# Performance work log

Hardware: AMD Instinct MI355X
Metric: run time of the kernel (lower is better)

## Reference

```python
import jax, jax.numpy as jnp
import numpy as np
from jax import lax

IOU_THRESHOLD = 0.5
TOP = 1000


def setup_inputs() -> dict:
    key = jax.random.key(0)
    k1, k2, k3, k4, k5 = jax.random.split(key, 5)
    B, P = 16, 20000
    # valid (x1, y1, x2, y2) boxes on an ~800x800 image
    x1 = jax.random.uniform(k1, (B, P)) * 800.0
    y1 = jax.random.uniform(k2, (B, P)) * 800.0
    w = jax.random.uniform(k3, (B, P)) * 200.0 + 1.0
    h = jax.random.uniform(k4, (B, P)) * 200.0 + 1.0
    reg = jnp.stack([x1, y1, x1 + w, y1 + h], axis=-1)  # [B, P, 4]
    cls = jax.random.normal(k5, (B, P))                  # [B, P]
    return {"reg": reg, "cls": cls}


def _pairwise_iou(boxes):
    """boxes: [B, N, 4] (x1,y1,x2,y2) -> IoU [B, N, N]."""
    a = boxes[:, :, None, :]  # [B, N, 1, 4]
    b = boxes[:, None, :, :]  # [B, 1, N, 4]
    xx1 = jnp.maximum(a[..., 0], b[..., 0])
    yy1 = jnp.maximum(a[..., 1], b[..., 1])
    xx2 = jnp.minimum(a[..., 2], b[..., 2])
    yy2 = jnp.minimum(a[..., 3], b[..., 3])
    inter = jnp.clip(xx2 - xx1, 0.0) * jnp.clip(yy2 - yy1, 0.0)
    area_a = (a[..., 2] - a[..., 0]) * (a[..., 3] - a[..., 1])
    area_b = (b[..., 2] - b[..., 0]) * (b[..., 3] - b[..., 1])
    return inter / (area_a + area_b - inter)


def reference(reg, cls):
    B = cls.shape[0]
    # sort by confidence descending, gather boxes, keep top
    order = jnp.argsort(-cls, axis=1)                      # [B, P]
    sorted_cls = jnp.take_along_axis(cls, order, axis=1)[:, :TOP]            # [B, N]
    sorted_reg = jnp.take_along_axis(reg, order[:, :, None], axis=1)[:, :TOP]  # [B, N, 4]
    N = sorted_cls.shape[1]

    iou = _pairwise_iou(sorted_reg)                        # [B, N, N]

    # sequential greedy suppression: if box i still kept, drop boxes with IoU>=thr
    def body(mask, i):
        keep_i = mask[:, i]                                # [B]
        tmp = iou[:, i, :] < IOU_THRESHOLD                 # [B, N]
        upd = (mask & tmp).at[:, i].set(True)
        new_mask = jnp.where(keep_i[:, None], upd, mask)
        return new_mask, None

    mask0 = jnp.ones((B, N), dtype=bool)
    mask, _ = lax.scan(body, mask0, jnp.arange(N))

    out_reg = jnp.where(mask[:, :, None], sorted_reg, 0.0)
    out_cls = jnp.where(mask, sorted_cls, 0.0)
    return out_reg, out_cls
```

## Files before the change

### kernel.cpp

```cpp
#include <hip/hip_runtime.h>
#include <stdint.h>

#define BATCH 16
#define NPTS  20000
#define TOPK  1000

__device__ __forceinline__ uint32_t key_desc(float f) {
    uint32_t u = __float_as_uint(f);
    uint32_t m = (u & 0x80000000u) ? ~u : (u | 0x80000000u);
    return ~m;
}

__device__ __forceinline__ float key_undo(uint32_t k) {
    uint32_t m = ~k;
    uint32_t u = (m & 0x80000000u) ? (m & 0x7FFFFFFFu) : ~m;
    return __uint_as_float(u);
}

__device__ __forceinline__ void digit_find(const uint32_t* hist, int* sh_r,
                                           uint32_t* sh_pfx, int shift, int tid) {
    if (tid < 64) {
        int r = *sh_r;
        uint32_t v0 = hist[4 * tid + 0], v1 = hist[4 * tid + 1];
        uint32_t v2 = hist[4 * tid + 2], v3 = hist[4 * tid + 3];
        uint32_t s = v0 + v1 + v2 + v3;
        uint32_t x = s;
        #pragma unroll
        for (int d = 1; d < 64; d <<= 1) {
            uint32_t t = __shfl_up(x, d);
            if (tid >= d) x += t;
        }
        uint32_t e0 = x - s;
        uint32_t e1 = e0 + v0, e2 = e1 + v1, e3 = e2 + v2, e4 = e3 + v3;
        uint32_t ur = (uint32_t)r;
        if (ur >= e0 && ur < e4) {
            int digit; uint32_t eSel;
            if      (ur < e1) { digit = 4 * tid + 0; eSel = e0; }
            else if (ur < e2) { digit = 4 * tid + 1; eSel = e1; }
            else if (ur < e3) { digit = 4 * tid + 2; eSel = e2; }
            else              { digit = 4 * tid + 3; eSel = e3; }
            *sh_r = r - (int)eSel;
            *sh_pfx |= ((uint32_t)digit << shift);
        }
    }
}

__global__ __launch_bounds__(1024) void topk_kernel(
    const float* __restrict__ reg, const float* __restrict__ cls,
    float4* __restrict__ ws_boxes, float* __restrict__ ws_cls)
{
    __shared__ uint32_t whist[16][256];
    __shared__ uint32_t merged[256];
    __shared__ uint32_t sh_kpfx;
    __shared__ uint32_t sh_ipfx;
    __shared__ int      sh_r;
    __shared__ int      sh_cnt;
    __shared__ uint64_t sel[1024];

    const int b    = blockIdx.x;
    const int tid  = threadIdx.x;
    const int wave = tid >> 6;
    const float* c = cls + (size_t)b * NPTS;

    if (tid == 0) { sh_r = TOPK - 1; sh_kpfx = 0; sh_ipfx = 0; sh_cnt = 0; }

    uint32_t kreg[20];
    #pragma unroll
    for (int j = 0; j < 20; ++j) {
        int p = tid + j * 1024;
        kreg[j] = (p < NPTS) ? key_desc(c[p]) : 0xFFFFFFFFu;
    }
    __syncthreads();

    uint32_t kpfx = 0, kmask = 0;
    for (int pass = 0; pass < 4; ++pass) {
        for (int i = tid; i < 16 * 256; i += 1024) ((uint32_t*)whist)[i] = 0;
        __syncthreads();
        const int shift = 24 - 8 * pass;
        #pragma unroll
        for (int j = 0; j < 20; ++j) {
            int p = tid + j * 1024;
            uint32_t k = kreg[j];
            if (p < NPTS && (k & kmask) == kpfx)
                atomicAdd(&whist[wave][(k >> shift) & 255], 1u);
        }
        __syncthreads();
        if (tid < 256) {
            uint32_t s = 0;
            #pragma unroll
            for (int w2 = 0; w2 < 16; ++w2) s += whist[w2][tid];
            merged[tid] = s;
        }
        __syncthreads();
        digit_find(merged, &sh_r, &sh_kpfx, shift, tid);
        __syncthreads();
        kpfx = sh_kpfx;
        kmask |= (0xFFu << shift);
    }
    const uint32_t kth = kpfx;
    const uint32_t kthcnt = merged[kth & 255];

    uint32_t ipfx = 0;
    if (kthcnt > 1) {
        uint32_t imask = 0;
        for (int pass = 0; pass < 2; ++pass) {
            for (int i = tid; i < 16 * 256; i += 1024) ((uint32_t*)whist)[i] = 0;
            __syncthreads();
            const int shift = 8 - 8 * pass;
            #pragma unroll
            for (int j = 0; j < 20; ++j) {
                int p = tid + j * 1024;
                if (p < NPTS && kreg[j] == kth && (((uint32_t)p) & imask) == ipfx)
                    atomicAdd(&whist[wave][((uint32_t)p >> shift) & 255], 1u);
            }
            __syncthreads();
            if (tid < 256) {
                uint32_t s = 0;
                #pragma unroll
                for (int w2 = 0; w2 < 16; ++w2) s += whist[w2][tid];
                merged[tid] = s;
            }
            __syncthreads();
            digit_find(merged, &sh_r, &sh_ipfx, shift, tid);
            __syncthreads();
            ipfx = sh_ipfx;
            imask |= (0xFFu << shift);
        }
    } else {
        ipfx = 0xFFFFFFFFu;
    }
    const uint64_t kthkey = ((uint64_t)kth << 32) | (uint64_t)ipfx;

    sel[tid] = ~0ull;
    __syncthreads();
    #pragma unroll
    for (int j = 0; j < 20; ++j) {
        int p = tid + j * 1024;
        if (p < NPTS) {
            uint64_t key = ((uint64_t)kreg[j] << 32) | (uint32_t)p;
            if (key <= kthkey) {
                int pos = atomicAdd(&sh_cnt, 1);
                sel[pos] = key;
            }
        }
    }
    __syncthreads();

    uint64_t v = sel[tid];
    for (int k = 2; k <= 1024; k <<= 1) {
        for (int j = k >> 1; j >= 64; j >>= 1) {
            __syncthreads();
            sel[tid] = v;
            __syncthreads();
            uint64_t o = sel[tid ^ j];
            bool upper = (tid & j) != 0;
            bool asc   = (tid & k) == 0;
            v = (upper == asc) ? (v > o ? v : o) : (v < o ? v : o);
        }
        int j0 = (k >> 1) < 64 ? (k >> 1) : 32;
        for (int j = j0; j >= 1; j >>= 1) {
            uint64_t o = __shfl_xor(v, j);
            bool upper = (tid & j) != 0;
            bool asc   = (tid & k) == 0;
            v = (upper == asc) ? (v > o ? v : o) : (v < o ? v : o);
        }
    }

    if (tid < TOPK) {
        int p = (int)(v & 0xFFFFFFFFull);
        ws_boxes[b * TOPK + tid] = ((const float4*)reg)[(size_t)b * NPTS + p];
        ws_cls[b * TOPK + tid] = key_undo((uint32_t)(v >> 32));
    }
}

__global__ __launch_bounds__(256) void iou_kernel(
    const float4* __restrict__ ws_boxes, uint32_t* __restrict__ suppT)
{
    __shared__ float4 boxes[TOPK];
    const int b     = blockIdx.y;
    const int chunk = blockIdx.x;
    const int tid   = threadIdx.x;
    for (int j = tid; j < TOPK; j += 256) boxes[j] = ws_boxes[b * TOPK + j];
    __syncthreads();

    const int lane = tid & 63;
    const int wave = tid >> 6;
    const int rbeg = chunk * 63;
    const int rend = (rbeg + 63 < TOPK) ? (rbeg + 63) : TOPK;
    uint32_t* t = suppT + (size_t)b * 32 * 1024;

    for (int i = rbeg + wave; i < rend; i += 4) {
        float4 a = boxes[i];
        float areaA = (a.z - a.x) * (a.w - a.y);
        uint64_t mine = 0;
        #pragma unroll
        for (int w = 0; w < 16; ++w) {
            int col = (w << 6) | lane;
            bool sup = false;
            if (col < TOPK) {
                float4 bb = boxes[col];
                float xx1 = fmaxf(a.x, bb.x);
                float yy1 = fmaxf(a.y, bb.y);
                float xx2 = fminf(a.z, bb.z);
                float yy2 = fminf(a.w, bb.w);
                float iw = fmaxf(xx2 - xx1, 0.0f);
                float ih = fmaxf(yy2 - yy1, 0.0f);
                float inter = iw * ih;
                float areaB = (bb.z - bb.x) * (bb.w - bb.y);
                float iou = inter / (areaA + areaB - inter);
                sup = (iou >= 0.5f);
            }
            uint64_t m = __ballot(sup);
            if (lane == w) mine = m;
        }
        if (lane < 16) {
            t[(2 * lane + 0) * 1024 + i] = (uint32_t)(mine & 0xFFFFFFFFull);
            t[(2 * lane + 1) * 1024 + i] = (uint32_t)(mine >> 32);
        }
    }
}

__global__ __launch_bounds__(64) void sweep_kernel(
    const uint32_t* __restrict__ suppT, const float4* __restrict__ ws_boxes,
    const float* __restrict__ ws_cls, float* __restrict__ out)
{
    const int b    = blockIdx.x;
    const int lane = threadIdx.x;
    const int myw  = lane & 31;
    const uint32_t* base = suppT + (size_t)b * 32 * 1024;

    uint32_t remv = 0, keptw = 0;
    uint4 dgA[8], clA[8], dgB[8], clB[8];

#define LOADG(W, DG, CL) { \
    const uint4* dp_ = (const uint4*)(base + (W) * 1024 + (W) * 32); \
    const uint4* cp_ = (const uint4*)(base + myw * 1024 + (W) * 32); \
    _Pragma("unroll") \
    for (int k_ = 0; k_ < 8; ++k_) { DG[k_] = dp_[k_]; CL[k_] = cp_[k_]; } }

#define STEP(D, C, BBIT) { \
    uint32_t live_ = (((~cur) >> (BBIT)) & 1u) & (uint32_t)((BBIT) < nb); \
    uint32_t msk_ = (uint32_t)0 - live_; \
    kmask |= (live_ << (BBIT)); \
    cur  |= (D) & msk_; \
    acc  |= (C) & msk_; }

#define PROC(W, DG, CL) { \
    const int nb = ((W) == 31) ? (TOPK - 31 * 32) : 32; \
    uint32_t cur = __shfl(remv, (W)); \
    uint32_t kmask = 0, acc = 0; \
    _Pragma("unroll") \
    for (int k_ = 0; k_ < 8; ++k_) { \
        STEP(DG[k_].x, CL[k_].x, 4 * k_ + 0); \
        STEP(DG[k_].y, CL[k_].y, 4 * k_ + 1); \
        STEP(DG[k_].z, CL[k_].z, 4 * k_ + 2); \
        STEP(DG[k_].w, CL[k_].w, 4 * k_ + 3); \
    } \
    remv |= acc; \
    if (myw == (W)) keptw = kmask; }

    LOADG(0, dgA, clA);
    #pragma unroll 1
    for (int w2 = 0; w2 < 16; ++w2) {
        const int wE = 2 * w2, wO = 2 * w2 + 1;
        LOADG(wO, dgB, clB);
        PROC(wE, dgA, clA);
        if (wO + 1 < 32) LOADG(wO + 1, dgA, clA);
        PROC(wO, dgB, clB);
    }

    __shared__ uint32_t skept[32];
    if (lane < 32) skept[lane] = keptw;
    __syncthreads();

    const float4* bx = ws_boxes + (size_t)b * TOPK;
    const float*  bc = ws_cls + (size_t)b * TOPK;
    float4* outr = (float4*)out + (size_t)b * TOPK;
    float*  outc = out + (size_t)BATCH * TOPK * 4 + (size_t)b * TOPK;
    for (int j = lane; j < TOPK; j += 64) {
        uint32_t keep = (skept[j >> 5] >> (j & 31)) & 1u;
        float4 v = bx[j];
        float cv = bc[j];
        outr[j] = keep ? v : make_float4(0.f, 0.f, 0.f, 0.f);
        outc[j] = keep ? cv : 0.0f;
    }
#undef LOADG
#undef STEP
#undef PROC
}

extern "C" void kernel_launch(void* const* d_in, const int* in_sizes, int n_in,
                              void* d_out, int out_size, void* d_ws, size_t ws_size,
                              hipStream_t stream) {
    (void)in_sizes; (void)n_in; (void)out_size; (void)ws_size;
    const float* reg = (const float*)d_in[0];
    const float* cls = (const float*)d_in[1];
    float* out = (float*)d_out;
    char* ws = (char*)d_ws;

    float4*   ws_boxes = (float4*)ws;
    float*    ws_cls   = (float*)(ws + 256000);
    uint32_t* suppT    = (uint32_t*)(ws + 320000);

    topk_kernel<<<dim3(BATCH), dim3(1024), 0, stream>>>(reg, cls, ws_boxes, ws_cls);
    iou_kernel<<<dim3(16, BATCH), dim3(256), 0, stream>>>(ws_boxes, suppT);
    sweep_kernel<<<dim3(BATCH), dim3(64), 0, stream>>>(suppT, ws_boxes, ws_cls, out);
}
```

Baseline: 74.70 us.

## Replace multi-pass 8-bit radix select with 11-bit histogram plus candidate refinement

Top-k threshold selection used to take four 8-bit radix passes over all keys, plus two index passes for ties. It now builds one 2048-bin histogram of the top 11 key bits, collects the keys in the threshold bin into a shared candidate list, and resolves the exact k-th key with a small second histogram or a single-wave rank selection. A bit-by-bit fallback covers the rare case of a very large bin. Wave-aggregated ballot atomics replace per-thread atomics when compacting the selected keys. The aim is fewer full passes and barriers over the 20k keys, at the cost of more code paths and extra shared memory.

```diff
diff --git a/kernel.cpp b/kernel.cpp
--- a/kernel.cpp
+++ b/kernel.cpp
@@ -4,6 +4,10 @@
 #define BATCH 16
 #define NPTS  20000
 #define TOPK  1000
+#define NKPT  20
+#define NBIN  2048
+#define NCOPY 4
+#define CANDCAP 2048
 
 __device__ __forceinline__ uint32_t key_desc(float f) {
     uint32_t u = __float_as_uint(f);
@@ -17,132 +21,183 @@
     return __uint_as_float(u);
 }
 
-__device__ __forceinline__ void digit_find(const uint32_t* hist, int* sh_r,
-                                           uint32_t* sh_pfx, int shift, int tid) {
-    if (tid < 64) {
-        int r = *sh_r;
-        uint32_t v0 = hist[4 * tid + 0], v1 = hist[4 * tid + 1];
-        uint32_t v2 = hist[4 * tid + 2], v3 = hist[4 * tid + 3];
-        uint32_t s = v0 + v1 + v2 + v3;
-        uint32_t x = s;
-        #pragma unroll
-        for (int d = 1; d < 64; d <<= 1) {
-            uint32_t t = __shfl_up(x, d);
-            if (tid >= d) x += t;
-        }
-        uint32_t e0 = x - s;
-        uint32_t e1 = e0 + v0, e2 = e1 + v1, e3 = e2 + v2, e4 = e3 + v3;
-        uint32_t ur = (uint32_t)r;
-        if (ur >= e0 && ur < e4) {
-            int digit; uint32_t eSel;
-            if      (ur < e1) { digit = 4 * tid + 0; eSel = e0; }
-            else if (ur < e2) { digit = 4 * tid + 1; eSel = e1; }
-            else if (ur < e3) { digit = 4 * tid + 2; eSel = e2; }
-            else              { digit = 4 * tid + 3; eSel = e3; }
-            *sh_r = r - (int)eSel;
-            *sh_pfx |= ((uint32_t)digit << shift);
-        }
-    }
+__device__ __forceinline__ void hist_scan_find(
+    uint32_t (*wh)[NBIN], uint32_t* wsum, uint32_t* wpre,
+    int* sh_T, int* sh_r, int* sh_binc,
+    int tid, int wave, int lane, uint32_t r)
+{
+    uint32_t m0 = 0, m1 = 0;
+    #pragma unroll
+    for (int cpy = 0; cpy < NCOPY; ++cpy) { m0 += wh[cpy][2*tid]; m1 += wh[cpy][2*tid+1]; }
+    uint32_t s = m0 + m1, x = s;
+    #pragma unroll
+    for (int d = 1; d < 64; d <<= 1) { uint32_t t = __shfl_up(x, d); if (lane >= d) x += t; }
+    if (lane == 63) wsum[wave] = x;
+    __syncthreads();
+    if (wave == 0 && lane < 16) {
+        uint32_t v = wsum[lane], y = v;
+        #pragma unroll
+        for (int d = 1; d < 16; d <<= 1) { uint32_t t = __shfl_up(y, d); if (lane >= d) y += t; }
+        wpre[lane] = y - v;
+    }
+    __syncthreads();
+    uint32_t e = wpre[wave] + (x - s);
+    if (r >= e && r < e + s) {
+        if (r < e + m0) { *sh_T = 2*tid;     *sh_r = (int)(r - e);      *sh_binc = (int)m0; }
+        else            { *sh_T = 2*tid + 1; *sh_r = (int)(r - e - m0); *sh_binc = (int)m1; }
+    }
+}
+
+__device__ __forceinline__ void push64(bool pred, uint64_t val, int* cntr,
+                                       uint64_t* list, int lane) {
+    uint64_t mask = __ballot(pred);
+    if (mask) {
+        int first = __ffsll((long long)mask) - 1;
+        int base = 0;
+        if (lane == first) base = atomicAdd(cntr, (int)__popcll(mask));
+        base = __shfl(base, first);
+        if (pred) {
+            int off = (int)__popcll(mask & ((1ull << lane) - 1ull));
+            list[base + off] = val;
+        }
+    }
+}
+
+__device__ __forceinline__ void wave_select(const uint64_t* lst, int n, int r,
+                                            uint64_t* out, int wave, int lane) {
+    if (wave == 0) {
+        uint64_t my = (lane < n) ? lst[lane] : ~0ull;
+        int rank = 0;
+        for (int i = 0; i < n; ++i) { uint64_t o = __shfl(my, i); if (o < my) rank++; }
+        if (lane < n && rank == r) *out = my;
+    }
+}
+
+__device__ uint64_t bit_search(const uint32_t* kreg, uint64_t known, uint64_t kmask,
+                               int startbit, uint32_t r, int* sh_c,
+                               int tid, int lane) {
+    for (int bit = startbit; bit >= 0; --bit) {
+        if (tid == 0) *sh_c = 0;
+        __syncthreads();
+        uint32_t local = 0;
+        #pragma unroll
+        for (int j = 0; j < NKPT; ++j) {
+            int p = tid + j * 1024;
+            uint64_t k64 = ((uint64_t)kreg[j] << 32) | (uint32_t)p;
+            if (p < NPTS && (k64 & kmask) == known && !((k64 >> bit) & 1ull)) local++;
+        }
+        #pragma unroll
+        for (int d = 1; d < 64; d <<= 1) local += __shfl_xor(local, d);
+        if (lane == 0 && local) atomicAdd(sh_c, (int)local);
+        __syncthreads();
+        uint32_t c0 = (uint32_t)*sh_c;
+        if (r >= c0) { known |= 1ull << bit; r -= c0; }
+        kmask |= 1ull << bit;
+        __syncthreads();
+    }
+    return known;
 }
 
 __global__ __launch_bounds__(1024) void topk_kernel(
     const float* __restrict__ reg, const float* __restrict__ cls,
     float4* __restrict__ ws_boxes, float* __restrict__ ws_cls)
 {
-    __shared__ uint32_t whist[16][256];
-    __shared__ uint32_t merged[256];
-    __shared__ uint32_t sh_kpfx;
-    __shared__ uint32_t sh_ipfx;
-    __shared__ int      sh_r;
-    __shared__ int      sh_cnt;
+    __shared__ uint32_t whist[NCOPY][NBIN];
+    __shared__ uint32_t wsum[16], wpre[16];
+    __shared__ int      sh_T, sh_r, sh_binc, sh_cnt;
+    __shared__ uint64_t sh_kthkey;
+    __shared__ uint64_t cand[CANDCAP];
+    __shared__ uint64_t cand2[64];
     __shared__ uint64_t sel[1024];
 
-    const int b    = blockIdx.x;
-    const int tid  = threadIdx.x;
-    const int wave = tid >> 6;
+    const int b = blockIdx.x, tid = threadIdx.x;
+    const int wave = tid >> 6, lane = tid & 63;
     const float* c = cls + (size_t)b * NPTS;
 
-    if (tid == 0) { sh_r = TOPK - 1; sh_kpfx = 0; sh_ipfx = 0; sh_cnt = 0; }
-
-    uint32_t kreg[20];
-    #pragma unroll
-    for (int j = 0; j < 20; ++j) {
+    uint32_t kreg[NKPT];
+    #pragma unroll
+    for (int j = 0; j < NKPT; ++j) {
         int p = tid + j * 1024;
         kreg[j] = (p < NPTS) ? key_desc(c[p]) : 0xFFFFFFFFu;
     }
-    __syncthreads();
-
-    uint32_t kpfx = 0, kmask = 0;
-    for (int pass = 0; pass < 4; ++pass) {
-        for (int i = tid; i < 16 * 256; i += 1024) ((uint32_t*)whist)[i] = 0;
-        __syncthreads();
-        const int shift = 24 - 8 * pass;
-        #pragma unroll
-        for (int j = 0; j < 20; ++j) {
+
+    #pragma unroll
+    for (int i = 0; i < NCOPY * NBIN / 1024; ++i) ((uint32_t*)whist)[tid + i * 1024] = 0;
+    __syncthreads();
+    #pragma unroll
+    for (int j = 0; j < NKPT; ++j) {
+        int p = tid + j * 1024;
+        if (p < NPTS) atomicAdd(&whist[wave >> 2][kreg[j] >> 21], 1u);
+    }
+    __syncthreads();
+    hist_scan_find(whist, wsum, wpre, &sh_T, &sh_r, &sh_binc, tid, wave, lane, TOPK - 1);
+    __syncthreads();
+    const int T1 = sh_T; int r = sh_r; const int cnt1 = sh_binc;
+    uint64_t known = (uint64_t)(uint32_t)T1 << 53;
+
+    if (cnt1 <= 64) {
+        if (tid == 0) sh_cnt = 0;
+        __syncthreads();
+        #pragma unroll
+        for (int j = 0; j < NKPT; ++j) {
             int p = tid + j * 1024;
-            uint32_t k = kreg[j];
-            if (p < NPTS && (k & kmask) == kpfx)
-                atomicAdd(&whist[wave][(k >> shift) & 255], 1u);
-        }
-        __syncthreads();
-        if (tid < 256) {
-            uint32_t s = 0;
-            #pragma unroll
-            for (int w2 = 0; w2 < 16; ++w2) s += whist[w2][tid];
-            merged[tid] = s;
-        }
-        __syncthreads();
-        digit_find(merged, &sh_r, &sh_kpfx, shift, tid);
-        __syncthreads();
-        kpfx = sh_kpfx;
-        kmask |= (0xFFu << shift);
-    }
-    const uint32_t kth = kpfx;
-    const uint32_t kthcnt = merged[kth & 255];
-
-    uint32_t ipfx = 0;
-    if (kthcnt > 1) {
-        uint32_t imask = 0;
-        for (int pass = 0; pass < 2; ++pass) {
-            for (int i = tid; i < 16 * 256; i += 1024) ((uint32_t*)whist)[i] = 0;
-            __syncthreads();
-            const int shift = 8 - 8 * pass;
-            #pragma unroll
-            for (int j = 0; j < 20; ++j) {
-                int p = tid + j * 1024;
-                if (p < NPTS && kreg[j] == kth && (((uint32_t)p) & imask) == ipfx)
-                    atomicAdd(&whist[wave][((uint32_t)p >> shift) & 255], 1u);
-            }
-            __syncthreads();
-            if (tid < 256) {
-                uint32_t s = 0;
-                #pragma unroll
-                for (int w2 = 0; w2 < 16; ++w2) s += whist[w2][tid];
-                merged[tid] = s;
-            }
-            __syncthreads();
-            digit_find(merged, &sh_r, &sh_ipfx, shift, tid);
-            __syncthreads();
-            ipfx = sh_ipfx;
-            imask |= (0xFFu << shift);
+            push64(p < NPTS && (kreg[j] >> 21) == (uint32_t)T1,
+                   ((uint64_t)kreg[j] << 32) | (uint32_t)p, &sh_cnt, cand2, lane);
+        }
+        __syncthreads();
+        wave_select(cand2, cnt1, r, &sh_kthkey, wave, lane);
+        __syncthreads();
+    } else if (cnt1 <= CANDCAP) {
+        if (tid == 0) sh_cnt = 0;
+        __syncthreads();
+        #pragma unroll
+        for (int j = 0; j < NKPT; ++j) {
+            int p = tid + j * 1024;
+            push64(p < NPTS && (kreg[j] >> 21) == (uint32_t)T1,
+                   ((uint64_t)kreg[j] << 32) | (uint32_t)p, &sh_cnt, cand, lane);
+        }
+        __syncthreads();
+        #pragma unroll
+        for (int i = 0; i < NCOPY * NBIN / 1024; ++i) ((uint32_t*)whist)[tid + i * 1024] = 0;
+        __syncthreads();
+        for (int i = tid; i < cnt1; i += 1024)
+            atomicAdd(&whist[wave >> 2][(uint32_t)((cand[i] >> 42) & 2047)], 1u);
+        __syncthreads();
+        hist_scan_find(whist, wsum, wpre, &sh_T, &sh_r, &sh_binc, tid, wave, lane, (uint32_t)r);
+        __syncthreads();
+        const int T2 = sh_T; r = sh_r; const int cnt2 = sh_binc;
+        known |= (uint64_t)(uint32_t)T2 << 42;
+        if (cnt2 <= 64) {
+            if (tid == 0) sh_cnt = 0;
+            __syncthreads();
+            for (int i = tid; i < cnt1; i += 1024)
+                push64(((cand[i] >> 42) & 2047) == (uint64_t)(uint32_t)T2,
+                       cand[i], &sh_cnt, cand2, lane);
+            __syncthreads();
+            wave_select(cand2, cnt2, r, &sh_kthkey, wave, lane);
+            __syncthreads();
+        } else {
+            uint64_t kk = bit_search(kreg, known, 0xFFFFFC0000000000ull, 41,
+                                     (uint32_t)r, &sh_cnt, tid, lane);
+            if (tid == 0) sh_kthkey = kk;
+            __syncthreads();
         }
     } else {
-        ipfx = 0xFFFFFFFFu;
-    }
-    const uint64_t kthkey = ((uint64_t)kth << 32) | (uint64_t)ipfx;
-
+        uint64_t kk = bit_search(kreg, known, 0xFFE0000000000000ull, 52,
+                                 (uint32_t)r, &sh_cnt, tid, lane);
+        if (tid == 0) sh_kthkey = kk;
+        __syncthreads();
+    }
+    const uint64_t kthkey = sh_kthkey;
+
+    if (tid == 0) sh_cnt = 0;
     sel[tid] = ~0ull;
     __syncthreads();
     #pragma unroll
-    for (int j = 0; j < 20; ++j) {
+    for (int j = 0; j < NKPT; ++j) {
         int p = tid + j * 1024;
-        if (p < NPTS) {
-            uint64_t key = ((uint64_t)kreg[j] << 32) | (uint32_t)p;
-            if (key <= kthkey) {
-                int pos = atomicAdd(&sh_cnt, 1);
-                sel[pos] = key;
-            }
-        }
+        uint64_t key = ((uint64_t)kreg[j] << 32) | (uint32_t)p;
+        push64(p < NPTS && key <= kthkey, key, &sh_cnt, sel, lane);
     }
     __syncthreads();
 
```

Result: faster. 72.77 us (-2.6%).
